# Kernel tuning notes

Hardware: AMD Instinct MI355X
Metric: run time of the kernel (lower is better)

Reference implementation:

```python
import jax, jax.numpy as jnp
import numpy as np

B, S, D_IN, D_OUT = 4, 2048, 4096, 4096
E = 32        # n_loras (number of LoRA experts)
R = 16        # per-expert rank; E*R == rmoe == 512
K = 2         # top_k
SCALING = 32.0 / 16.0  # lora_alpha / r (use_rslora=False)


def setup_inputs() -> dict:
    key = jax.random.key(0)
    ks = jax.random.split(key, 5)
    x = jax.random.normal(ks[0], (B, S, D_IN), dtype=jnp.float32)
    base_w = jax.random.normal(ks[1], (D_OUT, D_IN), dtype=jnp.float32) * 0.02
    gate_w = jax.random.normal(ks[2], (E, D_IN), dtype=jnp.float32) * 0.02
    lora_A = jax.random.normal(ks[3], (E * R, D_IN), dtype=jnp.float32) * 0.02
    lora_B = jax.random.normal(ks[4], (D_OUT, E * R), dtype=jnp.float32) * 0.02
    return {"x": x, "base_w": base_w, "gate_w": gate_w, "lora_A": lora_A, "lora_B": lora_B}


def reference(x, base_w, gate_w, lora_A, lora_B):
    # Base linear layer (nn.Linear, no bias)
    base = jnp.einsum('bsd,od->bso', x, base_w)

    # Gating: softmax over n_loras experts, top-k selection, renormalize
    logits = jnp.einsum('bsd,ed->bse', x, gate_w)              # [B,S,E]
    probs = jax.nn.softmax(logits, axis=-1)
    vals, idx = jax.lax.top_k(probs, K)                         # [B,S,K]
    vals = vals / jnp.sum(vals, axis=-1, keepdims=True)
    # Dense per-expert weight (zero for unselected experts)
    w = jnp.sum(jax.nn.one_hot(idx, E, dtype=x.dtype) * vals[..., None], axis=-2)  # [B,S,E]

    # Shared stacked LoRA: lora_A rows / lora_B cols are per-expert rank-R blocks
    ax = jnp.einsum('bsd,rd->bsr', x, lora_A).reshape(B, S, E, R)   # [B,S,E,R]
    b_blk = lora_B.T.reshape(E, R, D_OUT)                           # [E,R,out]
    delta = jnp.einsum('bser,ero->bso', ax * w[..., None], b_blk) * SCALING

    return base + delta
```

## Files before the change

### kernel.cpp

```cpp
#include <hip/hip_runtime.h>


#define D_IN   4096
#define D_OUT  4096
#define NTOK   8192
#define NE     32
#define RMOE   512
#define KCAT   4608
#define SCALING 2.0f

typedef unsigned short u16;
typedef __attribute__((ext_vector_type(4)))  float  f32x4;
typedef __attribute__((ext_vector_type(4)))  unsigned short u16x4;
typedef __attribute__((ext_vector_type(8)))  short  bf16x8;

__device__ __forceinline__ u16 f2bf(float f) {
  unsigned u = __float_as_uint(f);
  u += 0x7FFFu + ((u >> 16) & 1u);
  return (u16)(u >> 16);
}

__device__ __forceinline__ void gload16(const void* g, void* l) {
  __builtin_amdgcn_global_load_lds(
      (const __attribute__((address_space(1))) unsigned*)g,
      (__attribute__((address_space(3))) unsigned*)l, 16, 0, 0);
}

#define BAR() do { asm volatile("" ::: "memory"); \
                   __builtin_amdgcn_s_barrier();  \
                   asm volatile("" ::: "memory"); } while (0)
#define WAITV6() asm volatile("s_waitcnt vmcnt(6)" ::: "memory")
#define WAITV4() asm volatile("s_waitcnt vmcnt(4)" ::: "memory")
#define WAITV0() asm volatile("s_waitcnt vmcnt(0)" ::: "memory")

#define TT 32
#define KC 256

__global__ __launch_bounds__(256) void k_prep(
    const float* __restrict__ x, const float* __restrict__ gate_w,
    const float* __restrict__ base_w, const float* __restrict__ lora_B,
    const float* __restrict__ lora_A,
    float* __restrict__ wdense, u16* __restrict__ xb,
    u16* __restrict__ wb, u16* __restrict__ la)
{
  __shared__ float smem[2 * TT * KC];
  __shared__ float lgt[TT * 36];
  __shared__ int   e1s[TT]; __shared__ int   e2s[TT];
  __shared__ float w1s[TT]; __shared__ float w2s[TT];
  const int tid = threadIdx.x;

  if (blockIdx.x >= 256) {
    const int bid = blockIdx.x - 256;
    if (bid < D_OUT) {
      const float* src = base_w + (size_t)bid * D_IN;
      u16* dst = wb + (size_t)bid * KCAT;
#pragma unroll
      for (int i = 0; i < 4; ++i) {
        int c = tid + i * 256;
        f32x4 v = ((const f32x4*)src)[c];
        u16x4 h; h[0] = f2bf(v[0]); h[1] = f2bf(v[1]); h[2] = f2bf(v[2]); h[3] = f2bf(v[3]);
        ((u16x4*)dst)[c] = h;
      }
      if (tid < 128) {
        f32x4 v = ((const f32x4*)(lora_B + (size_t)bid * RMOE))[tid];
        u16x4 h; h[0] = f2bf(v[0]); h[1] = f2bf(v[1]); h[2] = f2bf(v[2]); h[3] = f2bf(v[3]);
        ((u16x4*)(dst + D_IN))[tid] = h;
      }
    } else {
      int r = bid - D_OUT;
      const float* src = lora_A + (size_t)r * D_IN;
      u16* dst = la + (size_t)r * D_IN;
#pragma unroll
      for (int i = 0; i < 4; ++i) {
        int c = tid + i * 256;
        f32x4 v = ((const f32x4*)src)[c];
        u16x4 h; h[0] = f2bf(v[0]); h[1] = f2bf(v[1]); h[2] = f2bf(v[2]); h[3] = f2bf(v[3]);
        ((u16x4*)dst)[c] = h;
      }
    }
    return;
  }

  float* xs = smem;
  float* gs = smem + TT * KC;
  const int lane = tid & 63, wave = tid >> 6;
  const int ks = lane >> 4, tg = (lane >> 2) & 3, eg = lane & 3;
  const int row0 = blockIdx.x * TT;
  const int kc0 = wave * 16 + ks * 4;

  float acc[8][8];
#pragma unroll
  for (int t = 0; t < 8; ++t)
#pragma unroll
    for (int e = 0; e < 8; ++e) acc[t][e] = 0.f;

  for (int kt = 0; kt < D_IN / KC; ++kt) {
    __syncthreads();
#pragma unroll
    for (int i = 0; i < 8; ++i) {
      int c = tid + i * 256;
      int tok = c >> 6, kq = c & 63;
      f32x4 v = ((const f32x4*)(x + (size_t)(row0 + tok) * D_IN + kt * KC))[kq];
      *(f32x4*)&xs[tok * KC + ((kq ^ (tok >> 3)) << 2)] = v;
      u16x4 h;
      h[0] = f2bf(v[0]); h[1] = f2bf(v[1]); h[2] = f2bf(v[2]); h[3] = f2bf(v[3]);
      ((u16x4*)(xb + (size_t)(row0 + tok) * KCAT + kt * KC))[kq] = h;
    }
#pragma unroll
    for (int i = 0; i < 8; ++i) {
      int c = tid + i * 256;
      int e = c >> 6, kq = c & 63;
      f32x4 v = ((const f32x4*)(gate_w + (size_t)e * D_IN + kt * KC))[kq];
      *(f32x4*)&gs[e * KC + ((kq ^ (e >> 3)) << 2)] = v;
    }
    __syncthreads();
#pragma unroll
    for (int j = 0; j < 4; ++j) {
      const int Kc = kc0 + j;
      f32x4 xv[8], gv[8];
#pragma unroll
      for (int t = 0; t < 8; ++t)
        xv[t] = *(const f32x4*)&xs[(tg * 8 + t) * KC + ((Kc ^ tg) << 2)];
#pragma unroll
      for (int e = 0; e < 8; ++e)
        gv[e] = *(const f32x4*)&gs[(eg * 8 + e) * KC + ((Kc ^ eg) << 2)];
#pragma unroll
      for (int t = 0; t < 8; ++t)
#pragma unroll
        for (int e = 0; e < 8; ++e)
#pragma unroll
          for (int m = 0; m < 4; ++m)
            acc[t][e] += xv[t][m] * gv[e][m];
    }
  }

#pragma unroll
  for (int t = 0; t < 8; ++t)
#pragma unroll
    for (int e = 0; e < 8; ++e) {
      float v = acc[t][e];
      v += __shfl_xor(v, 16);
      v += __shfl_xor(v, 32);
      acc[t][e] = v;
    }
  __syncthreads();
  float* red = smem;
  if (ks == 0) {
#pragma unroll
    for (int t = 0; t < 8; ++t)
#pragma unroll
      for (int e4 = 0; e4 < 8; e4 += 4) {
        f32x4 v = { acc[t][e4], acc[t][e4 + 1], acc[t][e4 + 2], acc[t][e4 + 3] };
        *(f32x4*)&red[(wave * 16 + tg * 4 + eg) * 64 + t * 8 + e4] = v;
      }
  }
  __syncthreads();
  {
    int tok = tid >> 3, e4 = (tid & 7) << 2;
    f32x4 s = {0.f, 0.f, 0.f, 0.f};
#pragma unroll
    for (int w = 0; w < 4; ++w)
      s += *(const f32x4*)&red[(w * 16 + (tok >> 3) * 4 + (e4 >> 3)) * 64 + (tok & 7) * 8 + (e4 & 7)];
    *(f32x4*)&lgt[tok * 36 + e4] = s;
  }
  __syncthreads();
  if (tid < TT) {
    float l1 = -1e30f; int e1 = 0;
    for (int e = 0; e < NE; ++e) { float v = lgt[tid * 36 + e]; if (v > l1) { l1 = v; e1 = e; } }
    float l2 = -1e30f; int e2 = 0;
    for (int e = 0; e < NE; ++e) { if (e == e1) continue; float v = lgt[tid * 36 + e]; if (v > l2) { l2 = v; e2 = e; } }
    float t = __expf(l2 - l1);
    float w2 = t / (1.f + t);
    e1s[tid] = e1; e2s[tid] = e2; w1s[tid] = 1.f - w2; w2s[tid] = w2;
  }
  __syncthreads();
#pragma unroll
  for (int i = 0; i < 4; ++i) {
    int c = tid + i * 256;
    int tok = c >> 5, e = c & 31;
    float v = (e == e1s[tok]) ? w1s[tok] : (e == e2s[tok]) ? w2s[tok] : 0.f;
    wdense[(size_t)(row0 + tok) * NE + e] = v;
  }
}

__global__ __launch_bounds__(256) void k_gemm_ax(
    const u16* __restrict__ A, const u16* __restrict__ La,
    const float* __restrict__ wdense, u16* __restrict__ xb)
{
  __shared__ u16 sh[36864];
  const int nwg = gridDim.x;
  int bid = blockIdx.x;
  int wg = (bid & 7) * (nwg >> 3) + (bid >> 3);
  const int tm = wg >> 2, tn = wg & 3;
  const int tid = threadIdx.x;
  const int lane = tid & 63, wn = tid >> 6;
  const int l15 = lane & 15, g = lane >> 4;
  const int row0 = tm * 64, col0 = tn * 128;

  size_t offA[2], offB[4]; int dA[2], dB[4];
#pragma unroll
  for (int i = 0; i < 2; ++i) {
    int c = tid + i * 256;
    int r = c >> 3, s = (c & 7) ^ (r & 7);
    offA[i] = (size_t)(row0 + r) * KCAT + s * 8;
    dA[i] = c * 8;
  }
#pragma unroll
  for (int i = 0; i < 4; ++i) {
    int c = tid + i * 256;
    int r = c >> 3, s = (c & 7) ^ (r & 7);
    offB[i] = (size_t)(col0 + r) * D_IN + s * 8;
    dB[i] = c * 8;
  }

#define STGAX(b, kt) do { \
    _Pragma("unroll") for (int i = 0; i < 2; ++i) \
      gload16(A  + offA[i] + (size_t)(kt) * 64, &sh[(b) * 12288 + dA[i]]); \
    _Pragma("unroll") for (int i = 0; i < 4; ++i) \
      gload16(La + offB[i] + (size_t)(kt) * 64, &sh[(b) * 12288 + 4096 + dB[i]]); } while (0)

  f32x4 acc[4][2];
#pragma unroll
  for (int i = 0; i < 4; ++i)
#pragma unroll
    for (int j = 0; j < 2; ++j) acc[i][j] = (f32x4){0.f, 0.f, 0.f, 0.f};

  STGAX(0, 0);
  STGAX(1, 1);
  WAITV6();
  BAR();

  const int swz = (g ^ (l15 & 7)) * 8;
  for (int kt = 0; kt < D_IN / 64; ++kt) {
    if (kt + 2 < D_IN / 64) STGAX((kt + 2) % 3, kt + 2);
    const u16* As_ = &sh[(kt % 3) * 12288];
    const u16* Bs_ = &sh[(kt % 3) * 12288 + 4096];
    bf16x8 af[4][2], bfr[2][2];
#pragma unroll
    for (int i = 0; i < 4; ++i) {
      int ixa = (i * 16 + l15) * 64 + swz;
      af[i][0] = *(const bf16x8*)&As_[ixa]; af[i][1] = *(const bf16x8*)&As_[ixa ^ 32];
    }
#pragma unroll
    for (int j = 0; j < 2; ++j) {
      int ixb = (wn * 32 + j * 16 + l15) * 64 + swz;
      bfr[j][0] = *(const bf16x8*)&Bs_[ixb]; bfr[j][1] = *(const bf16x8*)&Bs_[ixb ^ 32];
    }
    __builtin_amdgcn_s_setprio(1);
#pragma unroll
    for (int i = 0; i < 4; ++i)
#pragma unroll
      for (int j = 0; j < 2; ++j)
#pragma unroll
        for (int kk = 0; kk < 2; ++kk)
          acc[i][j] = __builtin_amdgcn_mfma_f32_16x16x32_bf16(af[i][kk], bfr[j][kk], acc[i][j], 0, 0, 0);
    __builtin_amdgcn_s_setprio(0);
    if (kt >= D_IN / 64 - 2) WAITV0(); else WAITV6();
    BAR();
  }
#undef STGAX

#pragma unroll
  for (int i = 0; i < 4; ++i) {
    int rbase = row0 + i * 16 + (g << 2);
#pragma unroll
    for (int j = 0; j < 2; ++j) {
      int cb = col0 + wn * 32 + j * 16 + l15;
#pragma unroll
      for (int q = 0; q < 4; ++q) {
        int trow = rbase + q;
        float wgt = wdense[(size_t)trow * NE + (cb >> 4)];
        xb[(size_t)trow * KCAT + D_IN + cb] = f2bf(acc[i][j][q] * wgt * SCALING);
      }
    }
  }
}

#define NT (KCAT / 64)

__global__ __launch_bounds__(512, 2) void k_gemm_main(
    const u16* __restrict__ A, const u16* __restrict__ Bw, float* __restrict__ C)
{
  __shared__ u16 sh[65536];

  const int tid  = threadIdx.x;
  const int lane = tid & 63;
  const int wv   = tid >> 6;
  const int wm   = wv >> 2;
  const int wn   = wv & 3;
  const int l15  = lane & 15, g = lane >> 4;

  const int nwg = gridDim.x;
  int bid = blockIdx.x;
  int wg = (bid & 7) * (nwg >> 3) + (bid >> 3);
  const int tn = wg & 15, tm = wg >> 4;

  const int rsw   = (g ^ (l15 & 7)) * 8;
  const int aBase = l15 * 64 + rsw;
  const int bBase = ((wn & 1) * 64 + l15) * 64 + rsw;

  const int c0 = tid, c1 = tid + 512;
  const int r0s = c0 >> 3, s0s = (c0 & 7) ^ (r0s & 7);
  const int r1s = c1 >> 3, s1s = (c1 & 7) ^ (r1s & 7);
  const size_t offc0 = (size_t)r0s * KCAT + s0s * 8;
  const size_t offc1 = (size_t)r1s * KCAT + s1s * 8;
  const u16* pA0a = A  + (size_t)(tm * 256 +   0) * KCAT + offc0;
  const u16* pA0b = A  + (size_t)(tm * 256 +   0) * KCAT + offc1;
  const u16* pA1a = A  + (size_t)(tm * 256 + 128) * KCAT + offc0;
  const u16* pA1b = A  + (size_t)(tm * 256 + 128) * KCAT + offc1;
  const u16* pB0a = Bw + (size_t)(tn * 256 +   0) * KCAT + offc0;
  const u16* pB0b = Bw + (size_t)(tn * 256 +   0) * KCAT + offc1;
  const u16* pB1a = Bw + (size_t)(tn * 256 + 128) * KCAT + offc0;
  const u16* pB1b = Bw + (size_t)(tn * 256 + 128) * KCAT + offc1;
  const int d0 = c0 * 8, d1 = c1 * 8;

#define STG(pa, pb, base) do { \
    gload16((pa), &sh[(base) + d0]); \
    gload16((pb), &sh[(base) + d1]); \
    (pa) += 64; (pb) += 64; } while (0)

#define MM4x2(MO, NO, AF, BF) do { \
    _Pragma("unroll") for (int m_ = 0; m_ < 4; ++m_) \
    _Pragma("unroll") for (int n_ = 0; n_ < 2; ++n_) \
    _Pragma("unroll") for (int kk_ = 0; kk_ < 2; ++kk_) \
      acc[m_ + (MO)][n_ + (NO)] = __builtin_amdgcn_mfma_f32_16x16x32_bf16( \
          AF[m_][kk_], BF[n_][kk_], acc[m_ + (MO)][n_ + (NO)], 0, 0, 0); } while (0)

  f32x4 acc[8][4];
#pragma unroll
  for (int i = 0; i < 8; ++i)
#pragma unroll
    for (int j = 0; j < 4; ++j) acc[i][j] = (f32x4){0.f, 0.f, 0.f, 0.f};

  STG(pA0a, pA0b,     0);
  STG(pB0a, pB0b, 16384);
  STG(pA1a, pA1b,  8192);
  STG(pB1a, pB1b, 24576);
  STG(pA0a, pA0b, 32768 +     0);
  STG(pB0a, pB0b, 32768 + 16384);
  WAITV4();
  BAR();

  bf16x8 aA[4][2], aB[4][2], bR[2][2];
  {
    const int shA = (wm << 13);
    const int shB = 16384 + ((wn >> 1) << 13);
#pragma unroll
    for (int m = 0; m < 4; ++m) {
      int ix = shA + aBase + m * 1024;
      aA[m][0] = *(const bf16x8*)&sh[ix]; aA[m][1] = *(const bf16x8*)&sh[ix ^ 32];
    }
#pragma unroll
    for (int n = 0; n < 2; ++n) {
      int ix = shB + bBase + n * 1024;
      bR[n][0] = *(const bf16x8*)&sh[ix]; bR[n][1] = *(const bf16x8*)&sh[ix ^ 32];
    }
  }

  for (int u = 0; u < NT; ++u) {
    const int cb = (u & 1) << 15;
    const int nb = cb ^ 32768;
    const int shA  = cb + (wm << 13);
    const int shB  = cb + 16384 + ((wn >> 1) << 13);
    const int shAn = nb + (wm << 13);
    const int shBn = nb + 16384 + ((wn >> 1) << 13);

    if (u < NT - 1) STG(pA1a, pA1b, nb + 8192);
#pragma unroll
    for (int m = 0; m < 4; ++m) {
      int ix = shA + aBase + (m + 4) * 1024;
      aB[m][0] = *(const bf16x8*)&sh[ix]; aB[m][1] = *(const bf16x8*)&sh[ix ^ 32];
    }
    BAR();
    __builtin_amdgcn_s_setprio(1);
    MM4x2(0, 0, aA, bR);
    __builtin_amdgcn_s_setprio(0);
    BAR();

    if (u < NT - 1) STG(pB1a, pB1b, nb + 24576);
    BAR();
    __builtin_amdgcn_s_setprio(1);
    MM4x2(4, 0, aB, bR);
    __builtin_amdgcn_s_setprio(0);
#pragma unroll
    for (int n = 0; n < 2; ++n) {
      int ix = shB + bBase + (n + 2) * 1024;
      bR[n][0] = *(const bf16x8*)&sh[ix]; bR[n][1] = *(const bf16x8*)&sh[ix ^ 32];
    }
    BAR();

    if (u < NT - 2) STG(pA0a, pA0b, cb + 0);
    BAR();
    __builtin_amdgcn_s_setprio(1);
    MM4x2(4, 2, aB, bR);
    __builtin_amdgcn_s_setprio(0);
    BAR();

    if (u < NT - 2) { STG(pB0a, pB0b, cb + 16384); WAITV4(); }
    else            { WAITV0(); }
    BAR();
    __builtin_amdgcn_s_setprio(1);
    MM4x2(0, 2, aA, bR);
    __builtin_amdgcn_s_setprio(0);
    if (u < NT - 1) {
#pragma unroll
      for (int m = 0; m < 4; ++m) {
        int ix = shAn + aBase + m * 1024;
        aA[m][0] = *(const bf16x8*)&sh[ix]; aA[m][1] = *(const bf16x8*)&sh[ix ^ 32];
      }
#pragma unroll
      for (int n = 0; n < 2; ++n) {
        int ix = shBn + bBase + n * 1024;
        bR[n][0] = *(const bf16x8*)&sh[ix]; bR[n][1] = *(const bf16x8*)&sh[ix ^ 32];
      }
    }
    BAR();
  }
#undef STG
#undef MM4x2

  const int crow0 = tm * 256 + wm * 128 + g * 4;
  const int ccol0 = tn * 256 + wn * 64 + l15;
#pragma unroll
  for (int mf = 0; mf < 8; ++mf)
#pragma unroll
    for (int n = 0; n < 4; ++n)
#pragma unroll
      for (int q = 0; q < 4; ++q)
        C[(size_t)(crow0 + mf * 16 + q) * D_OUT + ccol0 + n * 16] = acc[mf][n][q];
}

extern "C" void kernel_launch(void* const* d_in, const int* in_sizes, int n_in,
                              void* d_out, int out_size, void* d_ws, size_t ws_size,
                              hipStream_t stream) {
  const float* x      = (const float*)d_in[0];
  const float* base_w = (const float*)d_in[1];
  const float* gate_w = (const float*)d_in[2];
  const float* lora_A = (const float*)d_in[3];
  const float* lora_B = (const float*)d_in[4];
  float* out = (float*)d_out;

  char* ws = (char*)d_ws;
  u16* xb       = (u16*)ws;
  u16* wb       = (u16*)(ws + 75497472);
  u16* la       = (u16*)(ws + 75497472 + 37748736);
  float* wdense = (float*)(ws + 75497472 + 37748736 + 4194304);

  hipLaunchKernelGGL(k_prep,      dim3(256 + D_OUT + RMOE), dim3(256), 0, stream,
                     x, gate_w, base_w, lora_B, lora_A, wdense, xb, wb, la);
  hipLaunchKernelGGL(k_gemm_ax,   dim3((NTOK/64) * (RMOE/128)),  dim3(256), 0, stream,
                     xb, la, wdense, xb);
  hipLaunchKernelGGL(k_gemm_main, dim3((NTOK/256) * (D_OUT/256)), dim3(512), 0, stream,
                     xb, wb, out);
}
```

Baseline: 388.2 us.

## Split gating logits over K into four partial blocks and add top-2 kernel

The gate-logit prep now splits the K dimension into four quarters, so it launches 1024 token-chunk blocks instead of 256 and writes partial logits to a workspace buffer. A new small kernel sums the partials and does the top-2 selection and softmax-weight computation per token. Separately, the main GEMM loop reorders its MFMA quadrants and staging loads, adding an earlier vmcnt wait, to change how loads overlap with compute. This adds an extra launch and a round trip of partial logits through global memory.

```diff
diff --git a/kernel.cpp b/kernel.cpp
--- a/kernel.cpp
+++ b/kernel.cpp
@@ -40,17 +40,14 @@
     const float* __restrict__ x, const float* __restrict__ gate_w,
     const float* __restrict__ base_w, const float* __restrict__ lora_B,
     const float* __restrict__ lora_A,
-    float* __restrict__ wdense, u16* __restrict__ xb,
+    float* __restrict__ Pq, u16* __restrict__ xb,
     u16* __restrict__ wb, u16* __restrict__ la)
 {
   __shared__ float smem[2 * TT * KC];
-  __shared__ float lgt[TT * 36];
-  __shared__ int   e1s[TT]; __shared__ int   e2s[TT];
-  __shared__ float w1s[TT]; __shared__ float w2s[TT];
   const int tid = threadIdx.x;
 
-  if (blockIdx.x >= 256) {
-    const int bid = blockIdx.x - 256;
+  if (blockIdx.x >= 1024) {
+    const int bid = blockIdx.x - 1024;
     if (bid < D_OUT) {
       const float* src = base_w + (size_t)bid * D_IN;
       u16* dst = wb + (size_t)bid * KCAT;
@@ -83,9 +80,12 @@
 
   float* xs = smem;
   float* gs = smem + TT * KC;
+  const int b = blockIdx.x;
+  const int tc = b >> 2, kq4 = b & 3;
+  const int row0 = tc * TT;
+  const int kbase = kq4 * 1024;
   const int lane = tid & 63, wave = tid >> 6;
   const int ks = lane >> 4, tg = (lane >> 2) & 3, eg = lane & 3;
-  const int row0 = blockIdx.x * TT;
   const int kc0 = wave * 16 + ks * 4;
 
   float acc[8][8];
@@ -94,23 +94,23 @@
 #pragma unroll
     for (int e = 0; e < 8; ++e) acc[t][e] = 0.f;
 
-  for (int kt = 0; kt < D_IN / KC; ++kt) {
+  for (int kt = 0; kt < 4; ++kt) {
     __syncthreads();
 #pragma unroll
     for (int i = 0; i < 8; ++i) {
       int c = tid + i * 256;
       int tok = c >> 6, kq = c & 63;
-      f32x4 v = ((const f32x4*)(x + (size_t)(row0 + tok) * D_IN + kt * KC))[kq];
+      f32x4 v = ((const f32x4*)(x + (size_t)(row0 + tok) * D_IN + kbase + kt * KC))[kq];
       *(f32x4*)&xs[tok * KC + ((kq ^ (tok >> 3)) << 2)] = v;
       u16x4 h;
       h[0] = f2bf(v[0]); h[1] = f2bf(v[1]); h[2] = f2bf(v[2]); h[3] = f2bf(v[3]);
-      ((u16x4*)(xb + (size_t)(row0 + tok) * KCAT + kt * KC))[kq] = h;
+      ((u16x4*)(xb + (size_t)(row0 + tok) * KCAT + kbase + kt * KC))[kq] = h;
     }
 #pragma unroll
     for (int i = 0; i < 8; ++i) {
       int c = tid + i * 256;
       int e = c >> 6, kq = c & 63;
-      f32x4 v = ((const f32x4*)(gate_w + (size_t)e * D_IN + kt * KC))[kq];
+      f32x4 v = ((const f32x4*)(gate_w + (size_t)e * D_IN + kbase + kt * KC))[kq];
       *(f32x4*)&gs[e * KC + ((kq ^ (e >> 3)) << 2)] = v;
     }
     __syncthreads();
@@ -161,25 +161,46 @@
 #pragma unroll
     for (int w = 0; w < 4; ++w)
       s += *(const f32x4*)&red[(w * 16 + (tok >> 3) * 4 + (e4 >> 3)) * 64 + (tok & 7) * 8 + (e4 & 7)];
-    *(f32x4*)&lgt[tok * 36 + e4] = s;
-  }
-  __syncthreads();
-  if (tid < TT) {
-    float l1 = -1e30f; int e1 = 0;
-    for (int e = 0; e < NE; ++e) { float v = lgt[tid * 36 + e]; if (v > l1) { l1 = v; e1 = e; } }
-    float l2 = -1e30f; int e2 = 0;
-    for (int e = 0; e < NE; ++e) { if (e == e1) continue; float v = lgt[tid * 36 + e]; if (v > l2) { l2 = v; e2 = e; } }
-    float t = __expf(l2 - l1);
-    float w2 = t / (1.f + t);
-    e1s[tid] = e1; e2s[tid] = e2; w1s[tid] = 1.f - w2; w2s[tid] = w2;
-  }
-  __syncthreads();
-#pragma unroll
-  for (int i = 0; i < 4; ++i) {
-    int c = tid + i * 256;
-    int tok = c >> 5, e = c & 31;
-    float v = (e == e1s[tok]) ? w1s[tok] : (e == e2s[tok]) ? w2s[tok] : 0.f;
-    wdense[(size_t)(row0 + tok) * NE + e] = v;
+    *(f32x4*)&Pq[(size_t)kq4 * (NTOK * NE) + (size_t)(row0 + tok) * NE + e4] = s;
+  }
+}
+
+__global__ __launch_bounds__(256) void k_top2(
+    const float* __restrict__ Pq, float* __restrict__ wdense)
+{
+  const int t = blockIdx.x * 256 + threadIdx.x;
+  f32x4 s4[8];
+#pragma unroll
+  for (int i = 0; i < 8; ++i)
+    s4[i] = ((const f32x4*)(Pq + (size_t)t * NE))[i];
+#pragma unroll
+  for (int q = 1; q < 4; ++q)
+#pragma unroll
+    for (int i = 0; i < 8; ++i)
+      s4[i] += ((const f32x4*)(Pq + (size_t)q * (NTOK * NE) + (size_t)t * NE))[i];
+  float lg[32];
+#pragma unroll
+  for (int i = 0; i < 8; ++i) {
+    lg[i * 4 + 0] = s4[i][0]; lg[i * 4 + 1] = s4[i][1];
+    lg[i * 4 + 2] = s4[i][2]; lg[i * 4 + 3] = s4[i][3];
+  }
+  float l1 = -1e30f; int e1 = 0;
+#pragma unroll
+  for (int e = 0; e < NE; ++e) { if (lg[e] > l1) { l1 = lg[e]; e1 = e; } }
+  float l2 = -1e30f; int e2 = 0;
+#pragma unroll
+  for (int e = 0; e < NE; ++e) { if (e != e1 && lg[e] > l2) { l2 = lg[e]; e2 = e; } }
+  float tt = __expf(l2 - l1);
+  float w2 = tt / (1.f + tt), w1 = 1.f - w2;
+#pragma unroll
+  for (int i = 0; i < 8; ++i) {
+    f32x4 o;
+#pragma unroll
+    for (int j = 0; j < 4; ++j) {
+      int e = i * 4 + j;
+      o[j] = (e == e1) ? w1 : (e == e2) ? w2 : 0.f;
+    }
+    ((f32x4*)(wdense + (size_t)t * NE))[i] = o;
   }
 }
 
@@ -387,17 +408,10 @@
       int ix = shB + bBase + (n + 2) * 1024;
       bR[n][0] = *(const bf16x8*)&sh[ix]; bR[n][1] = *(const bf16x8*)&sh[ix ^ 32];
     }
+    WAITV4();
     BAR();
 
     if (u < NT - 2) STG(pA0a, pA0b, cb + 0);
-    BAR();
-    __builtin_amdgcn_s_setprio(1);
-    MM4x2(4, 2, aB, bR);
-    __builtin_amdgcn_s_setprio(0);
-    BAR();
-
-    if (u < NT - 2) { STG(pB0a, pB0b, cb + 16384); WAITV4(); }
-    else            { WAITV0(); }
     BAR();
     __builtin_amdgcn_s_setprio(1);
     MM4x2(0, 2, aA, bR);
@@ -408,6 +422,16 @@
         int ix = shAn + aBase + m * 1024;
         aA[m][0] = *(const bf16x8*)&sh[ix]; aA[m][1] = *(const bf16x8*)&sh[ix ^ 32];
       }
+    }
+    BAR();
+
+    if (u < NT - 2) { STG(pB0a, pB0b, cb + 16384); WAITV4(); }
+    else            { WAITV0(); }
+    BAR();
+    __builtin_amdgcn_s_setprio(1);
+    MM4x2(4, 2, aB, bR);
+    __builtin_amdgcn_s_setprio(0);
+    if (u < NT - 1) {
 #pragma unroll
       for (int n = 0; n < 2; ++n) {
         int ix = shBn + bBase + n * 1024;
@@ -445,9 +469,11 @@
   u16* wb       = (u16*)(ws + 75497472);
   u16* la       = (u16*)(ws + 75497472 + 37748736);
   float* wdense = (float*)(ws + 75497472 + 37748736 + 4194304);
-
-  hipLaunchKernelGGL(k_prep,      dim3(256 + D_OUT + RMOE), dim3(256), 0, stream,
-                     x, gate_w, base_w, lora_B, lora_A, wdense, xb, wb, la);
+  float* Pq     = (float*)(ws + 75497472 + 37748736 + 4194304 + 1048576);
+
+  hipLaunchKernelGGL(k_prep,      dim3(1024 + D_OUT + RMOE), dim3(256), 0, stream,
+                     x, gate_w, base_w, lora_B, lora_A, Pq, xb, wb, la);
+  hipLaunchKernelGGL(k_top2,      dim3(NTOK / 256), dim3(256), 0, stream, Pq, wdense);
   hipLaunchKernelGGL(k_gemm_ax,   dim3((NTOK/64) * (RMOE/128)),  dim3(256), 0, stream,
                      xb, la, wdense, xb);
   hipLaunchKernelGGL(k_gemm_main, dim3((NTOK/256) * (D_OUT/256)), dim3(512), 0, stream,
```

Measured after the change: 405.4 us. 4.4% more time.

## Unroll GEMM main loop by two and reorder MFMA quadrants for earlier fragment reloads

Applied to the files above, without the earlier changes.

Unrolls the double-buffered main loop by two so LDS buffer offsets become compile-time constants, and folds the per-warp LDS base into aBase/bBase. It also reorders the four MFMA quadrants so the next tile's A and B fragments are loaded from LDS right after the last use of each register set, overlapping those reads with the remaining MFMAs. An extra WAITV4 is added mid-tile. It assumes NT is even and raises register and instruction-cache pressure.

```diff
diff --git a/kernel.cpp b/kernel.cpp
--- a/kernel.cpp
+++ b/kernel.cpp
@@ -296,8 +296,8 @@
   const int tn = wg & 15, tm = wg >> 4;
 
   const int rsw   = (g ^ (l15 & 7)) * 8;
-  const int aBase = l15 * 64 + rsw;
-  const int bBase = ((wn & 1) * 64 + l15) * 64 + rsw;
+  const int aBase = (wm << 13) + l15 * 64 + rsw;
+  const int bBase = 16384 + ((wn >> 1) << 13) + ((wn & 1) * 64 + l15) * 64 + rsw;
 
   const int c0 = tid, c1 = tid + 512;
   const int r0s = c0 >> 3, s0s = (c0 & 7) ^ (r0s & 7);
@@ -326,6 +326,42 @@
       acc[m_ + (MO)][n_ + (NO)] = __builtin_amdgcn_mfma_f32_16x16x32_bf16( \
           AF[m_][kk_], BF[n_][kk_], acc[m_ + (MO)][n_ + (NO)], 0, 0, 0); } while (0)
 
+#define TILE(CB, C12, C34, CRF) do { \
+     \
+    if (C12) STG(pA1a, pA1b, ((CB) ^ 32768) + 8192); \
+    _Pragma("unroll") for (int m_ = 0; m_ < 4; ++m_) { \
+      int ix = (CB) + aBase + (m_ + 4) * 1024; \
+      aB[m_][0] = *(const bf16x8*)&sh[ix]; aB[m_][1] = *(const bf16x8*)&sh[ix ^ 32]; } \
+    BAR(); \
+    __builtin_amdgcn_s_setprio(1); MM4x2(0, 0, aA, bR); __builtin_amdgcn_s_setprio(0); \
+    BAR(); \
+     \
+    if (C12) STG(pB1a, pB1b, ((CB) ^ 32768) + 24576); \
+    BAR(); \
+    __builtin_amdgcn_s_setprio(1); MM4x2(4, 0, aB, bR); __builtin_amdgcn_s_setprio(0); \
+    _Pragma("unroll") for (int n_ = 0; n_ < 2; ++n_) { \
+      int ix = (CB) + bBase + (n_ + 2) * 1024; \
+      bR[n_][0] = *(const bf16x8*)&sh[ix]; bR[n_][1] = *(const bf16x8*)&sh[ix ^ 32]; } \
+    WAITV4(); \
+    BAR(); \
+     \
+    if (C34) STG(pA0a, pA0b, (CB) + 0); \
+    BAR(); \
+    __builtin_amdgcn_s_setprio(1); MM4x2(0, 2, aA, bR); __builtin_amdgcn_s_setprio(0); \
+    if (CRF) { _Pragma("unroll") for (int m_ = 0; m_ < 4; ++m_) { \
+      int ix = ((CB) ^ 32768) + aBase + m_ * 1024; \
+      aA[m_][0] = *(const bf16x8*)&sh[ix]; aA[m_][1] = *(const bf16x8*)&sh[ix ^ 32]; } } \
+    BAR(); \
+     \
+    if (C34) { STG(pB0a, pB0b, (CB) + 16384); WAITV4(); } else { WAITV0(); } \
+    BAR(); \
+    __builtin_amdgcn_s_setprio(1); MM4x2(4, 2, aB, bR); __builtin_amdgcn_s_setprio(0); \
+    if (CRF) { _Pragma("unroll") for (int n_ = 0; n_ < 2; ++n_) { \
+      int ix = ((CB) ^ 32768) + bBase + n_ * 1024; \
+      bR[n_][0] = *(const bf16x8*)&sh[ix]; bR[n_][1] = *(const bf16x8*)&sh[ix ^ 32]; } } \
+    BAR(); \
+  } while (0)
+
   f32x4 acc[8][4];
 #pragma unroll
   for (int i = 0; i < 8; ++i)
@@ -342,82 +378,25 @@
   BAR();
 
   bf16x8 aA[4][2], aB[4][2], bR[2][2];
-  {
-    const int shA = (wm << 13);
-    const int shB = 16384 + ((wn >> 1) << 13);
-#pragma unroll
-    for (int m = 0; m < 4; ++m) {
-      int ix = shA + aBase + m * 1024;
-      aA[m][0] = *(const bf16x8*)&sh[ix]; aA[m][1] = *(const bf16x8*)&sh[ix ^ 32];
-    }
-#pragma unroll
-    for (int n = 0; n < 2; ++n) {
-      int ix = shB + bBase + n * 1024;
-      bR[n][0] = *(const bf16x8*)&sh[ix]; bR[n][1] = *(const bf16x8*)&sh[ix ^ 32];
-    }
-  }
-
-  for (int u = 0; u < NT; ++u) {
-    const int cb = (u & 1) << 15;
-    const int nb = cb ^ 32768;
-    const int shA  = cb + (wm << 13);
-    const int shB  = cb + 16384 + ((wn >> 1) << 13);
-    const int shAn = nb + (wm << 13);
-    const int shBn = nb + 16384 + ((wn >> 1) << 13);
-
-    if (u < NT - 1) STG(pA1a, pA1b, nb + 8192);
-#pragma unroll
-    for (int m = 0; m < 4; ++m) {
-      int ix = shA + aBase + (m + 4) * 1024;
-      aB[m][0] = *(const bf16x8*)&sh[ix]; aB[m][1] = *(const bf16x8*)&sh[ix ^ 32];
-    }
-    BAR();
-    __builtin_amdgcn_s_setprio(1);
-    MM4x2(0, 0, aA, bR);
-    __builtin_amdgcn_s_setprio(0);
-    BAR();
-
-    if (u < NT - 1) STG(pB1a, pB1b, nb + 24576);
-    BAR();
-    __builtin_amdgcn_s_setprio(1);
-    MM4x2(4, 0, aB, bR);
-    __builtin_amdgcn_s_setprio(0);
-#pragma unroll
-    for (int n = 0; n < 2; ++n) {
-      int ix = shB + bBase + (n + 2) * 1024;
-      bR[n][0] = *(const bf16x8*)&sh[ix]; bR[n][1] = *(const bf16x8*)&sh[ix ^ 32];
-    }
-    BAR();
-
-    if (u < NT - 2) STG(pA0a, pA0b, cb + 0);
-    BAR();
-    __builtin_amdgcn_s_setprio(1);
-    MM4x2(4, 2, aB, bR);
-    __builtin_amdgcn_s_setprio(0);
-    BAR();
-
-    if (u < NT - 2) { STG(pB0a, pB0b, cb + 16384); WAITV4(); }
-    else            { WAITV0(); }
-    BAR();
-    __builtin_amdgcn_s_setprio(1);
-    MM4x2(0, 2, aA, bR);
-    __builtin_amdgcn_s_setprio(0);
-    if (u < NT - 1) {
-#pragma unroll
-      for (int m = 0; m < 4; ++m) {
-        int ix = shAn + aBase + m * 1024;
-        aA[m][0] = *(const bf16x8*)&sh[ix]; aA[m][1] = *(const bf16x8*)&sh[ix ^ 32];
-      }
-#pragma unroll
-      for (int n = 0; n < 2; ++n) {
-        int ix = shBn + bBase + n * 1024;
-        bR[n][0] = *(const bf16x8*)&sh[ix]; bR[n][1] = *(const bf16x8*)&sh[ix ^ 32];
-      }
-    }
-    BAR();
+#pragma unroll
+  for (int m = 0; m < 4; ++m) {
+    int ix = aBase + m * 1024;
+    aA[m][0] = *(const bf16x8*)&sh[ix]; aA[m][1] = *(const bf16x8*)&sh[ix ^ 32];
+  }
+#pragma unroll
+  for (int n = 0; n < 2; ++n) {
+    int ix = bBase + n * 1024;
+    bR[n][0] = *(const bf16x8*)&sh[ix]; bR[n][1] = *(const bf16x8*)&sh[ix ^ 32];
+  }
+
+  for (int i = 0; i < NT / 2; ++i) {
+    const bool nl = (i < NT / 2 - 1);
+    TILE(0,     true, nl, true);
+    TILE(32768, nl,   nl, nl);
   }
 #undef STG
 #undef MM4x2
+#undef TILE
 
   const int crow0 = tm * 256 + wm * 128 + g * 4;
   const int ccol0 = tn * 256 + wn * 64 + l15;
```

Result: slower. 503.4 us (+29.7%).
